# Kernel optimization log

Hardware: AMD Instinct MI355X
Metric: run time of the kernel (lower is better)

The kernel has to match this reference:

```python
import jax, jax.numpy as jnp
import numpy as np


def setup_inputs() -> dict:
    key = jax.random.key(0)
    nX, time_steps, T = 1024, 256, 10
    u0 = jax.random.normal(key, (nX, nX), dtype=jnp.float32)
    # learnable scalar diffusivity; 2e-4 keeps gamma <= 0.25 (stable scheme)
    alpha = jnp.asarray(2e-4, dtype=jnp.float32)
    return {"u0": u0, "alpha": alpha, "T": T, "nX": nX, "time_steps": time_steps}


def reference(u0, alpha, T, nX, time_steps):
    delta_x = 6.0 / (nX - 1)
    delta_t = T / (time_steps - 1)
    gamma = alpha * delta_t / delta_x ** 2

    # Torch code writes u0 at t=0, then zeroes all four boundaries for every t.
    u_init = jnp.zeros_like(u0).at[1:-1, 1:-1].set(u0[1:-1, 1:-1])

    def step(u, _):
        # 5-point Laplacian stencil on the interior; boundaries stay 0
        lap = (u[2:, 1:-1] + u[:-2, 1:-1] + u[1:-1, 2:] + u[1:-1, :-2]
               - 4.0 * u[1:-1, 1:-1])
        un = jnp.zeros_like(u).at[1:-1, 1:-1].set(gamma * lap + u[1:-1, 1:-1])
        return un, un

    _, us = jax.lax.scan(step, u_init, None, length=time_steps - 1)
    # u: [time_steps, nX, nX]
    return jnp.concatenate([u_init[None], us], axis=0)
```

## Files before the change

kernel.cpp:

```cpp
#include <hip/hip_runtime.h>
#include <math.h>


#define CORE 64
#define HALO 16
#define REG  96
#define NQ   (REG / 4)
#define TPB  1024
#define NIT  (94 * NQ)

__global__ __launch_bounds__(256)
void heat_init(const float* __restrict__ u0, float* __restrict__ out, int nX) {
    const int row = blockIdx.x;
    const int j   = threadIdx.x;
    const int nq  = nX >> 2;
    float4* dst = reinterpret_cast<float4*>(out + (size_t)row * nX);
    if (row == 0 || row == nX - 1) {
        dst[j] = make_float4(0.f, 0.f, 0.f, 0.f);
        return;
    }
    const float4* src = reinterpret_cast<const float4*>(u0 + (size_t)row * nX);
    float4 v = src[j];
    if (j == 0)      v.x = 0.f;
    if (j == nq - 1) v.w = 0.f;
    dst[j] = v;
}

__device__ __forceinline__ void step_quad(const float* __restrict__ bc,
                                          float* __restrict__ bn,
                                          float* __restrict__ of,
                                          int it, float4& c, float gamma,
                                          int o_r, int o_c, int nX) {
    const int r = 1 + it / NQ;
    const int q = it % NQ;
    const float4 u4 = reinterpret_cast<const float4*>(bc)[(r - 1) * NQ + q];
    const float4 d4 = reinterpret_cast<const float4*>(bc)[(r + 1) * NQ + q];
    const float lf = bc[r * REG + 4 * q - 1];
    const float rt = bc[r * REG + 4 * q + 4];

    float4 o;
    o.x = c.x + gamma * (u4.x + d4.x + lf  + c.y - 4.f * c.x);
    o.y = c.y + gamma * (u4.y + d4.y + c.x + c.z - 4.f * c.y);
    o.z = c.z + gamma * (u4.z + d4.z + c.y + c.w - 4.f * c.z);
    o.w = c.w + gamma * (u4.w + d4.w + c.z + rt  - 4.f * c.w);

    const int gr  = o_r + r;
    const int gc0 = o_c + 4 * q;
    if (gr <= 0 || gr >= nX - 1) {
        o = make_float4(0.f, 0.f, 0.f, 0.f);
    } else {
        if (gc0     <= 0 || gc0     >= nX - 1) o.x = 0.f;
        if (gc0 + 1 <= 0 || gc0 + 1 >= nX - 1) o.y = 0.f;
        if (gc0 + 2 <= 0 || gc0 + 2 >= nX - 1) o.z = 0.f;
        if (gc0 + 3 <= 0 || gc0 + 3 >= nX - 1) o.w = 0.f;
    }
    reinterpret_cast<float4*>(bn)[r * NQ + q] = o;

    if (r >= HALO && r < HALO + CORE && q >= HALO / 4 && q < (REG - HALO) / 4) {
        *reinterpret_cast<float4*>(of + (size_t)gr * nX + gc0) = o;
    }
    c = o;
}

__global__ __launch_bounds__(TPB)
void heat_fused(const float* __restrict__ uin,
                float* __restrict__ out,
                int t_base, int k, int nX, int time_steps,
                const float* __restrict__ alpha_p,
                const int* __restrict__ T_p) {
    __shared__ float buf[2][REG * REG];

    const int tid = threadIdx.x;
    const int gb  = nX / CORE;
    const int bx  = blockIdx.x % gb;
    const int by  = blockIdx.x / gb;
    const int o_r = by * CORE - HALO;
    const int o_c = bx * CORE - HALO;

    const float alpha = *alpha_p;
    const float Tf    = (float)(*T_p);
    const float dx    = 6.0f / (float)(nX - 1);
    const float dt    = Tf / (float)(time_steps - 1);
    const float gamma = alpha * dt / (dx * dx);

    for (int idx = tid; idx < REG * REG; idx += TPB) {
        const int r  = idx / REG, c = idx % REG;
        const int gr = o_r + r,  gc = o_c + c;
        float v = 0.f;
        if (gr >= 0 && gr < nX && gc >= 0 && gc < nX)
            v = uin[(size_t)gr * nX + gc];
        buf[0][idx] = v;
    }
    asm volatile("s_waitcnt lgkmcnt(0)" ::: "memory");
    __builtin_amdgcn_s_barrier();
    __builtin_amdgcn_sched_barrier(0);

    float4 c0 = reinterpret_cast<const float4*>(buf[0])[NQ + tid];
    float4 c1 = reinterpret_cast<const float4*>(buf[0])[NQ + tid + TPB];
    const bool has2 = (tid + 2 * TPB) < NIT;
    float4 c2 = make_float4(0.f, 0.f, 0.f, 0.f);
    if (has2) c2 = reinterpret_cast<const float4*>(buf[0])[NQ + tid + 2 * TPB];

    int cur = 0;
    for (int s = 0; s < k; ++s) {
        const float* __restrict__ bc = buf[cur];
        float*       __restrict__ bn = buf[cur ^ 1];
        float* of = out + (size_t)(t_base + s + 1) * nX * nX;

        step_quad(bc, bn, of, tid,           c0, gamma, o_r, o_c, nX);
        step_quad(bc, bn, of, tid + TPB,     c1, gamma, o_r, o_c, nX);
        if (has2)
            step_quad(bc, bn, of, tid + 2 * TPB, c2, gamma, o_r, o_c, nX);

        asm volatile("s_waitcnt lgkmcnt(0)" ::: "memory");
        __builtin_amdgcn_s_barrier();
        __builtin_amdgcn_sched_barrier(0);
        asm volatile("" ::: "memory");
        cur ^= 1;
    }
}

extern "C" void kernel_launch(void* const* d_in, const int* in_sizes, int n_in,
                              void* d_out, int out_size, void* d_ws, size_t ws_size,
                              hipStream_t stream) {
    const float* u0      = (const float*)d_in[0];
    const float* alpha_p = (const float*)d_in[1];
    const int*   T_p     = (const int*)d_in[2];

    const int n0 = in_sizes[0];
    const int nX = (int)(sqrtf((float)n0) + 0.5f);
    const int ts = out_size / n0;

    float* out = (float*)d_out;
    const int gb = nX / CORE;
    const int nblocks = gb * gb;

    heat_init<<<nX, nX / 4, 0, stream>>>(u0, out, nX);

    for (int t = 0; t < ts - 1; t += HALO) {
        const int k = min(HALO, ts - 1 - t);
        heat_fused<<<nblocks, TPB, 0, stream>>>(out + (size_t)t * n0, out,
                                                t, k, nX, ts, alpha_p, T_p);
    }
}
```

Before: 330.5 us.

## Fuse init into first stencil launch, pad shared rows, precompute slot masks

Removes the separate init kernel: the first fused launch reads u0 directly, zeroes boundaries while loading the tile, and writes the t=0 frame from the core region. Shared-memory rows are padded to 100 floats, which changes LDS bank mapping. Per-slot addresses, store predicates and boundary masks are precomputed once, so the inner loop applies a multiply mask instead of recomputing branches. The main cost is still the output write bandwidth, so the benefit is mostly one fewer launch and less per-step integer work.

```diff
diff --git a/kernel.cpp b/kernel.cpp
--- a/kernel.cpp
+++ b/kernel.cpp
@@ -5,70 +5,53 @@
 #define CORE 64
 #define HALO 16
 #define REG  96
-#define NQ   (REG / 4)
+#define PAD  100
 #define TPB  1024
-#define NIT  (94 * NQ)
+#define NIT  (94 * 24)
 
-__global__ __launch_bounds__(256)
-void heat_init(const float* __restrict__ u0, float* __restrict__ out, int nX) {
-    const int row = blockIdx.x;
-    const int j   = threadIdx.x;
-    const int nq  = nX >> 2;
-    float4* dst = reinterpret_cast<float4*>(out + (size_t)row * nX);
-    if (row == 0 || row == nX - 1) {
-        dst[j] = make_float4(0.f, 0.f, 0.f, 0.f);
-        return;
-    }
-    const float4* src = reinterpret_cast<const float4*>(u0 + (size_t)row * nX);
-    float4 v = src[j];
-    if (j == 0)      v.x = 0.f;
-    if (j == nq - 1) v.w = 0.f;
-    dst[j] = v;
+__device__ __forceinline__ void slot_init(int it, int o_r, int o_c, int nX,
+                                          int& a, size_t& so, bool& st, float4& m) {
+    const int r = 1 + it / 24;
+    const int q = it % 24;
+    a = r * PAD + 4 * q;
+    const int gr  = o_r + r;
+    const int gc0 = o_c + 4 * q;
+    so = (size_t)gr * nX + gc0;
+    st = (r >= HALO && r < HALO + CORE && q >= HALO / 4 && q < (REG - HALO) / 4);
+    const bool rin = (gr > 0 && gr < nX - 1);
+    m.x = (rin && gc0     > 0 && gc0     < nX - 1) ? 1.f : 0.f;
+    m.y = (rin && gc0 + 1 > 0 && gc0 + 1 < nX - 1) ? 1.f : 0.f;
+    m.z = (rin && gc0 + 2 > 0 && gc0 + 2 < nX - 1) ? 1.f : 0.f;
+    m.w = (rin && gc0 + 3 > 0 && gc0 + 3 < nX - 1) ? 1.f : 0.f;
 }
 
-__device__ __forceinline__ void step_quad(const float* __restrict__ bc,
-                                          float* __restrict__ bn,
-                                          float* __restrict__ of,
-                                          int it, float4& c, float gamma,
-                                          int o_r, int o_c, int nX) {
-    const int r = 1 + it / NQ;
-    const int q = it % NQ;
-    const float4 u4 = reinterpret_cast<const float4*>(bc)[(r - 1) * NQ + q];
-    const float4 d4 = reinterpret_cast<const float4*>(bc)[(r + 1) * NQ + q];
-    const float lf = bc[r * REG + 4 * q - 1];
-    const float rt = bc[r * REG + 4 * q + 4];
-
+__device__ __forceinline__ void step_one(const float* __restrict__ bc,
+                                         float* __restrict__ bn,
+                                         float* __restrict__ of,
+                                         int a, size_t so, bool st,
+                                         const float4& m, float4& c, float gamma) {
+    const float4 u4 = *reinterpret_cast<const float4*>(bc + a - PAD);
+    const float4 d4 = *reinterpret_cast<const float4*>(bc + a + PAD);
+    const float lf = bc[a - 1];
+    const float rt = bc[a + 4];
     float4 o;
-    o.x = c.x + gamma * (u4.x + d4.x + lf  + c.y - 4.f * c.x);
-    o.y = c.y + gamma * (u4.y + d4.y + c.x + c.z - 4.f * c.y);
-    o.z = c.z + gamma * (u4.z + d4.z + c.y + c.w - 4.f * c.z);
-    o.w = c.w + gamma * (u4.w + d4.w + c.z + rt  - 4.f * c.w);
-
-    const int gr  = o_r + r;
-    const int gc0 = o_c + 4 * q;
-    if (gr <= 0 || gr >= nX - 1) {
-        o = make_float4(0.f, 0.f, 0.f, 0.f);
-    } else {
-        if (gc0     <= 0 || gc0     >= nX - 1) o.x = 0.f;
-        if (gc0 + 1 <= 0 || gc0 + 1 >= nX - 1) o.y = 0.f;
-        if (gc0 + 2 <= 0 || gc0 + 2 >= nX - 1) o.z = 0.f;
-        if (gc0 + 3 <= 0 || gc0 + 3 >= nX - 1) o.w = 0.f;
-    }
-    reinterpret_cast<float4*>(bn)[r * NQ + q] = o;
-
-    if (r >= HALO && r < HALO + CORE && q >= HALO / 4 && q < (REG - HALO) / 4) {
-        *reinterpret_cast<float4*>(of + (size_t)gr * nX + gc0) = o;
-    }
+    o.x = m.x * (c.x + gamma * (u4.x + d4.x + lf  + c.y - 4.f * c.x));
+    o.y = m.y * (c.y + gamma * (u4.y + d4.y + c.x + c.z - 4.f * c.y));
+    o.z = m.z * (c.z + gamma * (u4.z + d4.z + c.y + c.w - 4.f * c.z));
+    o.w = m.w * (c.w + gamma * (u4.w + d4.w + c.z + rt  - 4.f * c.w));
+    *reinterpret_cast<float4*>(bn + a) = o;
+    if (st) *reinterpret_cast<float4*>(of + so) = o;
     c = o;
 }
 
 __global__ __launch_bounds__(TPB)
-void heat_fused(const float* __restrict__ uin,
+void heat_fused(const float* __restrict__ src,
                 float* __restrict__ out,
-                int t_base, int k, int nX, int time_steps,
+                int t_base, int k, int nX, int first,
+                int time_steps,
                 const float* __restrict__ alpha_p,
                 const int* __restrict__ T_p) {
-    __shared__ float buf[2][REG * REG];
+    __shared__ float buf[2][REG * PAD];
 
     const int tid = threadIdx.x;
     const int gb  = nX / CORE;
@@ -83,23 +66,31 @@
     const float dt    = Tf / (float)(time_steps - 1);
     const float gamma = alpha * dt / (dx * dx);
 
-    for (int idx = tid; idx < REG * REG; idx += TPB) {
-        const int r  = idx / REG, c = idx % REG;
-        const int gr = o_r + r,  gc = o_c + c;
+    for (int idx = tid; idx < REG * PAD; idx += TPB) {
+        const int r = idx / PAD, c = idx % PAD;
+        const int gr = o_r + r, gc = o_c + c;
         float v = 0.f;
-        if (gr >= 0 && gr < nX && gc >= 0 && gc < nX)
-            v = uin[(size_t)gr * nX + gc];
+        if (c < REG && gr > 0 && gr < nX - 1 && gc > 0 && gc < nX - 1)
+            v = src[(size_t)gr * nX + gc];
         buf[0][idx] = v;
+        if (first && r >= HALO && r < HALO + CORE && c >= HALO && c < HALO + CORE)
+            out[(size_t)gr * nX + gc] = v;
     }
     asm volatile("s_waitcnt lgkmcnt(0)" ::: "memory");
     __builtin_amdgcn_s_barrier();
     __builtin_amdgcn_sched_barrier(0);
 
-    float4 c0 = reinterpret_cast<const float4*>(buf[0])[NQ + tid];
-    float4 c1 = reinterpret_cast<const float4*>(buf[0])[NQ + tid + TPB];
+    int a0, a1, a2 = PAD; size_t so0, so1, so2 = 0; bool st0, st1, st2 = false;
+    float4 m0, m1, m2;
+    slot_init(tid,           o_r, o_c, nX, a0, so0, st0, m0);
+    slot_init(tid + TPB,     o_r, o_c, nX, a1, so1, st1, m1);
     const bool has2 = (tid + 2 * TPB) < NIT;
+    if (has2) slot_init(tid + 2 * TPB, o_r, o_c, nX, a2, so2, st2, m2);
+
+    float4 c0 = *reinterpret_cast<const float4*>(&buf[0][a0]);
+    float4 c1 = *reinterpret_cast<const float4*>(&buf[0][a1]);
     float4 c2 = make_float4(0.f, 0.f, 0.f, 0.f);
-    if (has2) c2 = reinterpret_cast<const float4*>(buf[0])[NQ + tid + 2 * TPB];
+    if (has2) c2 = *reinterpret_cast<const float4*>(&buf[0][a2]);
 
     int cur = 0;
     for (int s = 0; s < k; ++s) {
@@ -107,15 +98,13 @@
         float*       __restrict__ bn = buf[cur ^ 1];
         float* of = out + (size_t)(t_base + s + 1) * nX * nX;
 
-        step_quad(bc, bn, of, tid,           c0, gamma, o_r, o_c, nX);
-        step_quad(bc, bn, of, tid + TPB,     c1, gamma, o_r, o_c, nX);
-        if (has2)
-            step_quad(bc, bn, of, tid + 2 * TPB, c2, gamma, o_r, o_c, nX);
+        step_one(bc, bn, of, a0, so0, st0, m0, c0, gamma);
+        step_one(bc, bn, of, a1, so1, st1, m1, c1, gamma);
+        if (has2) step_one(bc, bn, of, a2, so2, st2, m2, c2, gamma);
 
         asm volatile("s_waitcnt lgkmcnt(0)" ::: "memory");
         __builtin_amdgcn_s_barrier();
         __builtin_amdgcn_sched_barrier(0);
-        asm volatile("" ::: "memory");
         cur ^= 1;
     }
 }
@@ -135,11 +124,11 @@
     const int gb = nX / CORE;
     const int nblocks = gb * gb;
 
-    heat_init<<<nX, nX / 4, 0, stream>>>(u0, out, nX);
-
     for (int t = 0; t < ts - 1; t += HALO) {
         const int k = min(HALO, ts - 1 - t);
-        heat_fused<<<nblocks, TPB, 0, stream>>>(out + (size_t)t * n0, out,
-                                                t, k, nX, ts, alpha_p, T_p);
+        const float* src = (t == 0) ? u0 : out + (size_t)t * n0;
+        heat_fused<<<nblocks, TPB, 0, stream>>>(src, out, t, k, nX,
+                                                (t == 0) ? 1 : 0, ts,
+                                                alpha_p, T_p);
     }
 }
```

After: 343.2 us. 3.8% more time.
